# Optimization experiments

Measured on AMD Instinct MI355X. Metric: run time of the kernel, lower is better.

Reference implementation:

```python
import jax, jax.numpy as jnp
import numpy as np

N = 50000   # nodes
E = 800000  # edges
B = 64      # graphs in batch
IN = 128    # in_features
HID = 64    # hidden_channels
H = 4       # head_count
C = 10      # out_classes
NEG = 0.2   # leaky relu negative slope
EPS = 1e-5  # batchnorm eps (eval mode, running mean 0 / var 1)


def _gat(x, edge_index, W, a_src, a_dst, b):
    """PyG GATConv (add_self_loops=False, concat=True), eval mode (no dropout)."""
    Hh, F = a_src.shape
    xW = (x @ W).reshape(-1, Hh, F)                       # [N,H,F]
    src, dst = edge_index[0], edge_index[1]
    e = (jnp.einsum('nhf,hf->nh', xW, a_src)[src]
         + jnp.einsum('nhf,hf->nh', xW, a_dst)[dst])      # [E,H]
    e = jnp.where(e > 0, e, NEG * e)                      # leaky relu
    m = jax.ops.segment_max(e, dst, num_segments=N)       # per-dst max
    m = jnp.where(jnp.isfinite(m), m, 0.0)
    p = jnp.exp(e - m[dst])
    denom = jax.ops.segment_sum(p, dst, num_segments=N)
    alpha = p / jnp.maximum(denom[dst], 1e-16)            # edge softmax over dst
    out = jax.ops.segment_sum(alpha[:, :, None] * xW[src], dst, num_segments=N)
    return out.reshape(-1, Hh * F) + b


def _bn_relu(y, g, be):
    # BatchNorm1d in eval mode with running_mean=0, running_var=1, then ReLU
    return jax.nn.relu(g * y / jnp.sqrt(1.0 + EPS) + be)


def setup_inputs():
    key = jax.random.key(0)
    ks = jax.random.split(key, 24)
    s = lambda k, shape: (jax.random.normal(k, shape, jnp.float32) * 0.05)
    z = lambda shape: jnp.zeros(shape, jnp.float32)
    o = lambda shape: jnp.ones(shape, jnp.float32)
    return {
        'acc_flag': 0,
        'x': jax.random.normal(ks[0], (N, IN), jnp.float32),
        'edge_index': jax.random.randint(ks[1], (2, E), 0, N),
        'batch': jnp.sort(jax.random.randint(ks[2], (N,), 0, B)),
        # layer 1: GATConv(IN -> HID, heads=H, concat)
        'W1': s(ks[3], (IN, H * HID)), 'a_src1': s(ks[4], (H, HID)), 'a_dst1': s(ks[5], (H, HID)), 'b1': z((H * HID,)),
        # proj: GATConv(H*HID -> HID, heads=1) + BN
        'W2': s(ks[6], (H * HID, HID)), 'a_src2': s(ks[7], (1, HID)), 'a_dst2': s(ks[8], (1, HID)), 'b2': z((HID,)), 'g2': o((HID,)), 'be2': z((HID,)),
        # block 1
        'W3': s(ks[9], (HID, HID)), 'a_src3': s(ks[10], (1, HID)), 'a_dst3': s(ks[11], (1, HID)), 'b3': z((HID,)), 'g3': o((HID,)), 'be3': z((HID,)),
        # block 2
        'W4': s(ks[12], (HID, HID)), 'a_src4': s(ks[13], (1, HID)), 'a_dst4': s(ks[14], (1, HID)), 'b4': z((HID,)), 'g4': o((HID,)), 'be4': z((HID,)),
        # MLP head
        'Wh1': s(ks[15], (HID, 128)), 'bh1': z((128,)),
        'Wh2': s(ks[16], (128, C)), 'bh2': z((C,)),
    }


def reference(acc_flag, x, edge_index, batch,
              W1, a_src1, a_dst1, b1,
              W2, a_src2, a_dst2, b2, g2, be2,
              W3, a_src3, a_dst3, b3, g3, be3,
              W4, a_src4, a_dst4, b4, g4, be4,
              Wh1, bh1, Wh2, bh2):
    # hardware GAT layer + ReLU (relu applied twice in original -> idempotent)
    x1 = jax.nn.relu(_gat(x, edge_index, W1, a_src1, a_dst1, b1))   # [N, H*HID]
    # projection block: residual base is zeros (shape mismatch H*HID vs HID)
    h = _bn_relu(_gat(x1, edge_index, W2, a_src2, a_dst2, b2), g2, be2)
    # residual blocks (shapes match -> x + relu(bn(y)))
    h = h + _bn_relu(_gat(h, edge_index, W3, a_src3, a_dst3, b3), g3, be3)
    h = h + _bn_relu(_gat(h, edge_index, W4, a_src4, a_dst4, b4), g4, be4)
    # global mean pool over graphs
    pooled = jax.ops.segment_sum(h, batch, num_segments=B)
    cnt = jnp.maximum(jax.ops.segment_sum(jnp.ones((N,), h.dtype), batch, num_segments=B), 1.0)
    hp = pooled / cnt[:, None]                                      # [B, HID]
    # MLP head
    return jax.nn.relu(hp @ Wh1 + bh1) @ Wh2 + bh2                  # [B, C]
```

## Files before the change

kernel.cpp:

```cpp
#include <hip/hip_runtime.h>

#define N_NODES 50000
#define N_EDGES 800000
#define N_GRAPHS 64
#define F_IN 128
#define F_HID 64
#define N_HEADS 4
#define N_CLASSES 10
#define NEG_SLOPE 0.2f
#define BN_RSQ 0.9999950000374997f

typedef __bf16 bf16x8 __attribute__((ext_vector_type(8)));
typedef float floatx4 __attribute__((ext_vector_type(4)));

__device__ __forceinline__ float lrelu(float v) { return v > 0.0f ? v : NEG_SLOPE * v; }

__device__ __forceinline__ float b2f(unsigned short u) {
    return __uint_as_float(((unsigned int)u) << 16);
}
__device__ __forceinline__ unsigned short f2b(float f) {
    unsigned int u = __float_as_uint(f);
    return (unsigned short)((u + 0x7fffu + ((u >> 16) & 1u)) >> 16);
}
__device__ __forceinline__ float blo(unsigned int d) { return __uint_as_float(d << 16); }
__device__ __forceinline__ float bhi(unsigned int d) { return __uint_as_float(d & 0xffff0000u); }

__global__ void k_deg(const int* __restrict__ ei, int* __restrict__ deg) {
    int e = blockIdx.x * blockDim.x + threadIdx.x;
    if (e < N_EDGES) atomicAdd(&deg[ei[N_EDGES + e]], 1);
}

__global__ void k_offs(const int* __restrict__ deg, int* __restrict__ offs,
                       int* __restrict__ total) {
    int i = blockIdx.x * blockDim.x + threadIdx.x;
    int lane = threadIdx.x & 63;
    int v = (i < N_NODES) ? deg[i] : 0;
    int incl = v;
    for (int o = 1; o < 64; o <<= 1) {
        int t = __shfl_up(incl, o);
        if (lane >= o) incl += t;
    }
    int wtot = __shfl(incl, 63);
    int base = 0;
    if (lane == 0) base = atomicAdd(total, wtot);
    base = __shfl(base, 0);
    if (i < N_NODES) offs[i] = base + incl - v;
}

__global__ void k_fill(const int* __restrict__ ei, const int* __restrict__ offs,
                       int* __restrict__ cur, int* __restrict__ csr_src) {
    int e = blockIdx.x * blockDim.x + threadIdx.x;
    if (e < N_EDGES) {
        int d = ei[N_EDGES + e];
        int pos = offs[d] + atomicAdd(&cur[d], 1);
        csr_src[pos] = ei[e];
    }
}

__global__ void k_bounds(const int* __restrict__ batch, int* __restrict__ bounds) {
    int g = threadIdx.x;
    if (g > N_GRAPHS) return;
    int lo = 0, hi = N_NODES;
    while (lo < hi) {
        int mid = (lo + hi) >> 1;
        if (batch[mid] < g) lo = mid + 1; else hi = mid;
    }
    bounds[g] = lo;
}

__global__ void k_prepw(const float* __restrict__ W, unsigned short* __restrict__ Wt,
                        int K, int N) {
    int i = blockIdx.x * blockDim.x + threadIdx.x;
    if (i < K * N) {
        int k = i / N, n = i % N;
        Wt[n * K + k] = f2b(W[i]);
    }
}

template <int K, int N, int HEADS, bool AF32>
__global__ __launch_bounds__(256) void k_mgemm(const void* __restrict__ Ap,
                                               const unsigned short* __restrict__ Bt,
                                               const float* __restrict__ asrc,
                                               const float* __restrict__ adst,
                                               unsigned short* __restrict__ out,
                                               float* __restrict__ es,
                                               float* __restrict__ ed, int rows) {
    constexpr int LDP = K + 8;
    __shared__ unsigned short As[64 * LDP];
    const int tid = threadIdx.x;
    const int r0 = blockIdx.x * 64;
    if (AF32) {
        const float* A = (const float*)Ap;
        for (int i = tid; i < 16 * K; i += 256) {
            int r = i / (K / 4), c4 = i % (K / 4);
            int row = r0 + r;
            float4 v = (row < rows) ? *(const float4*)&A[(size_t)row * K + c4 * 4]
                                    : make_float4(0.f, 0.f, 0.f, 0.f);
            ushort4 u;
            u.x = f2b(v.x); u.y = f2b(v.y); u.z = f2b(v.z); u.w = f2b(v.w);
            *(ushort4*)&As[r * LDP + c4 * 4] = u;
        }
    } else {
        const unsigned short* A = (const unsigned short*)Ap;
        for (int i = tid; i < 8 * K; i += 256) {
            int r = i / (K / 8), c8 = i % (K / 8);
            int row = r0 + r;
            uint4 v;
            if (row < rows) v = *(const uint4*)&A[(size_t)row * K + c8 * 8];
            else { v.x = v.y = v.z = v.w = 0; }
            *(uint4*)&As[r * LDP + c8 * 8] = v;
        }
    }
    __syncthreads();
    const int w = tid >> 6, lane = tid & 63;
    const int quad = lane >> 4, l16 = lane & 15;
    const int gr0 = r0 + w * 16 + quad * 4;
    bf16x8 afrag[K / 32];
#pragma unroll
    for (int kk = 0; kk < K / 32; ++kk)
        afrag[kk] = *(const bf16x8*)&As[(w * 16 + l16) * LDP + kk * 32 + quad * 8];
    float sacc[4] = {0.f, 0.f, 0.f, 0.f};
    float dacc[4] = {0.f, 0.f, 0.f, 0.f};
#pragma unroll 1
    for (int ct = 0; ct < N / 16; ++ct) {
        floatx4 acc = {0.f, 0.f, 0.f, 0.f};
#pragma unroll
        for (int kk = 0; kk < K / 32; ++kk) {
            const bf16x8 bfrag =
                *(const bf16x8*)&Bt[(size_t)(ct * 16 + l16) * K + kk * 32 + quad * 8];
            acc = __builtin_amdgcn_mfma_f32_16x16x32_bf16(afrag[kk], bfrag, acc, 0, 0, 0);
        }
        const int gc = ct * 16 + l16;
        const int hh = gc >> 6;
        const float av = asrc[gc & (64 * HEADS > N ? N - 1 : 63) + (hh << 6) - (hh << 6)
                              ];
        (void)av;
        {
            const int f = gc & 63;
            const float as = asrc[hh * 64 + f];
            const float ad = adst[hh * 64 + f];
#pragma unroll
            for (int rg = 0; rg < 4; ++rg) {
                sacc[rg] = fmaf(acc[rg], as, sacc[rg]);
                dacc[rg] = fmaf(acc[rg], ad, dacc[rg]);
            }
        }
#pragma unroll
        for (int rg = 0; rg < 4; ++rg) {
            int gr = gr0 + rg;
            if (gr < rows) out[(size_t)gr * N + gc] = f2b(acc[rg]);
        }
        if ((ct & 3) == 3) {
#pragma unroll
            for (int rg = 0; rg < 4; ++rg) {
                float s = sacc[rg], d = dacc[rg];
                for (int o = 1; o < 16; o <<= 1) {
                    s += __shfl_xor(s, o);
                    d += __shfl_xor(d, o);
                }
                if (l16 == 0) {
                    int gr = gr0 + rg;
                    if (gr < rows) {
                        es[(size_t)gr * HEADS + hh] = s;
                        ed[(size_t)gr * HEADS + hh] = d;
                    }
                }
                sacc[rg] = 0.f;
                dacc[rg] = 0.f;
            }
        }
    }
}

__global__ __launch_bounds__(256) void k_gat1(
    const unsigned short* __restrict__ xW, const float* __restrict__ es, const float* __restrict__ ed,
    const int* __restrict__ offs, const int* __restrict__ deg, const int* __restrict__ csr,
    const float* __restrict__ bias, unsigned short* __restrict__ out) {
    __shared__ float ps[4][256];
    __shared__ int sbuf[4][64];
    const int wv = threadIdx.x >> 6;
    const int lane = threadIdx.x & 63;
    const int n = blockIdx.x * 4 + wv;
    if (n >= N_NODES) return;
    const int off = offs[n];
    const int dg = deg[n];
    const float4 edv = *(const float4*)&ed[n * 4];
    const int t = lane & 15, grp = lane >> 4, hq = t >> 2;

    float acc[16];
#pragma unroll
    for (int k = 0; k < 16; ++k) acc[k] = 0.f;
    float d0 = 0.f, d1 = 0.f, d2 = 0.f, d3 = 0.f;

    for (int base = 0; base < dg; base += 64) {
        const int idx = base + lane;
        int s_l = 0;
        float p0 = 0.f, p1 = 0.f, p2 = 0.f, p3 = 0.f;
        if (idx < dg) {
            s_l = csr[off + idx];
            const float4 ev = *(const float4*)&es[s_l * 4];
            p0 = __expf(lrelu(ev.x + edv.x));
            p1 = __expf(lrelu(ev.y + edv.y));
            p2 = __expf(lrelu(ev.z + edv.z));
            p3 = __expf(lrelu(ev.w + edv.w));
        }
        d0 += p0; d1 += p1; d2 += p2; d3 += p3;
        *(float4*)&ps[wv][lane * 4] = make_float4(p0, p1, p2, p3);
        sbuf[wv][lane] = s_l;
        const int cnt = min(64, dg - base);
        const int cntR = (cnt + 7) & ~7;
        for (int j4 = 0; j4 < cntR; j4 += 8) {
            const int ja = j4 + grp;
            const int jb = ja + 4;
            const float pa = ps[wv][ja * 4 + hq];
            const float pb = ps[wv][jb * 4 + hq];
            const int sa = sbuf[wv][ja];
            const int sb = sbuf[wv][jb];
            const uint4 a0 = *(const uint4*)&xW[(size_t)sa * 256 + t * 16];
            const uint4 a1 = *(const uint4*)&xW[(size_t)sa * 256 + t * 16 + 8];
            const uint4 b0 = *(const uint4*)&xW[(size_t)sb * 256 + t * 16];
            const uint4 b1 = *(const uint4*)&xW[(size_t)sb * 256 + t * 16 + 8];
            acc[0]  = fmaf(pa, blo(a0.x), acc[0]);
            acc[1]  = fmaf(pa, bhi(a0.x), acc[1]);
            acc[2]  = fmaf(pa, blo(a0.y), acc[2]);
            acc[3]  = fmaf(pa, bhi(a0.y), acc[3]);
            acc[4]  = fmaf(pa, blo(a0.z), acc[4]);
            acc[5]  = fmaf(pa, bhi(a0.z), acc[5]);
            acc[6]  = fmaf(pa, blo(a0.w), acc[6]);
            acc[7]  = fmaf(pa, bhi(a0.w), acc[7]);
            acc[8]  = fmaf(pa, blo(a1.x), acc[8]);
            acc[9]  = fmaf(pa, bhi(a1.x), acc[9]);
            acc[10] = fmaf(pa, blo(a1.y), acc[10]);
            acc[11] = fmaf(pa, bhi(a1.y), acc[11]);
            acc[12] = fmaf(pa, blo(a1.z), acc[12]);
            acc[13] = fmaf(pa, bhi(a1.z), acc[13]);
            acc[14] = fmaf(pa, blo(a1.w), acc[14]);
            acc[15] = fmaf(pa, bhi(a1.w), acc[15]);
            acc[0]  = fmaf(pb, blo(b0.x), acc[0]);
            acc[1]  = fmaf(pb, bhi(b0.x), acc[1]);
            acc[2]  = fmaf(pb, blo(b0.y), acc[2]);
            acc[3]  = fmaf(pb, bhi(b0.y), acc[3]);
            acc[4]  = fmaf(pb, blo(b0.z), acc[4]);
            acc[5]  = fmaf(pb, bhi(b0.z), acc[5]);
            acc[6]  = fmaf(pb, blo(b0.w), acc[6]);
            acc[7]  = fmaf(pb, bhi(b0.w), acc[7]);
            acc[8]  = fmaf(pb, blo(b1.x), acc[8]);
            acc[9]  = fmaf(pb, bhi(b1.x), acc[9]);
            acc[10] = fmaf(pb, blo(b1.y), acc[10]);
            acc[11] = fmaf(pb, bhi(b1.y), acc[11]);
            acc[12] = fmaf(pb, blo(b1.z), acc[12]);
            acc[13] = fmaf(pb, bhi(b1.z), acc[13]);
            acc[14] = fmaf(pb, blo(b1.w), acc[14]);
            acc[15] = fmaf(pb, bhi(b1.w), acc[15]);
        }
    }
#pragma unroll
    for (int k = 0; k < 16; ++k) {
        acc[k] += __shfl_xor(acc[k], 16);
        acc[k] += __shfl_xor(acc[k], 32);
    }
    for (int o = 1; o < 64; o <<= 1) {
        d0 += __shfl_xor(d0, o);
        d1 += __shfl_xor(d1, o);
        d2 += __shfl_xor(d2, o);
        d3 += __shfl_xor(d3, o);
    }
    if (grp == 0) {
        const float dsel = hq == 0 ? d0 : hq == 1 ? d1 : hq == 2 ? d2 : d3;
        const float inv = 1.0f / fmaxf(dsel, 1e-16f);
#pragma unroll
        for (int k4 = 0; k4 < 16; k4 += 4) {
            const int c = t * 16 + k4;
            const float4 bv = *(const float4*)&bias[c];
            ushort4 o4;
            o4.x = f2b(fmaxf(fmaf(acc[k4 + 0], inv, bv.x), 0.f));
            o4.y = f2b(fmaxf(fmaf(acc[k4 + 1], inv, bv.y), 0.f));
            o4.z = f2b(fmaxf(fmaf(acc[k4 + 2], inv, bv.z), 0.f));
            o4.w = f2b(fmaxf(fmaf(acc[k4 + 3], inv, bv.w), 0.f));
            *(ushort4*)&out[(size_t)n * 256 + c] = o4;
        }
    }
}

template <bool RES>
__global__ __launch_bounds__(256) void k_gatL(
    const unsigned short* __restrict__ xW, const float* __restrict__ es, const float* __restrict__ ed,
    const int* __restrict__ offs, const int* __restrict__ deg, const int* __restrict__ csr,
    const float* __restrict__ bias, const float* __restrict__ gam, const float* __restrict__ bet,
    float* __restrict__ h, unsigned short* __restrict__ hb) {
    __shared__ float ps[4][64];
    __shared__ int sbuf[4][64];
    const int wv = threadIdx.x >> 6;
    const int lane = threadIdx.x & 63;
    const int n = blockIdx.x * 4 + wv;
    if (n >= N_NODES) return;
    const int off = offs[n];
    const int dg = deg[n];
    const float edn = ed[n];
    const int t = lane & 7, grp = lane >> 3;

    float acc[8];
#pragma unroll
    for (int k = 0; k < 8; ++k) acc[k] = 0.f;
    float dsum = 0.f;

    for (int base = 0; base < dg; base += 64) {
        const int idx = base + lane;
        int s_l = 0;
        float p_l = 0.f;
        if (idx < dg) {
            s_l = csr[off + idx];
            p_l = __expf(lrelu(es[s_l] + edn));
        }
        dsum += p_l;
        ps[wv][lane] = p_l;
        sbuf[wv][lane] = s_l;
        const int cnt = min(64, dg - base);
        const int cntR = (cnt + 15) & ~15;
        for (int j8 = 0; j8 < cntR; j8 += 16) {
            const int ja = j8 + grp;
            const int jb = ja + 8;
            const float pa = ps[wv][ja];
            const float pb = ps[wv][jb];
            const int sa = sbuf[wv][ja];
            const int sb = sbuf[wv][jb];
            const uint4 a = *(const uint4*)&xW[(size_t)sa * 64 + t * 8];
            const uint4 b = *(const uint4*)&xW[(size_t)sb * 64 + t * 8];
            acc[0] = fmaf(pa, blo(a.x), acc[0]);
            acc[1] = fmaf(pa, bhi(a.x), acc[1]);
            acc[2] = fmaf(pa, blo(a.y), acc[2]);
            acc[3] = fmaf(pa, bhi(a.y), acc[3]);
            acc[4] = fmaf(pa, blo(a.z), acc[4]);
            acc[5] = fmaf(pa, bhi(a.z), acc[5]);
            acc[6] = fmaf(pa, blo(a.w), acc[6]);
            acc[7] = fmaf(pa, bhi(a.w), acc[7]);
            acc[0] = fmaf(pb, blo(b.x), acc[0]);
            acc[1] = fmaf(pb, bhi(b.x), acc[1]);
            acc[2] = fmaf(pb, blo(b.y), acc[2]);
            acc[3] = fmaf(pb, bhi(b.y), acc[3]);
            acc[4] = fmaf(pb, blo(b.z), acc[4]);
            acc[5] = fmaf(pb, bhi(b.z), acc[5]);
            acc[6] = fmaf(pb, blo(b.w), acc[6]);
            acc[7] = fmaf(pb, bhi(b.w), acc[7]);
        }
    }
#pragma unroll
    for (int k = 0; k < 8; ++k) {
        acc[k] += __shfl_xor(acc[k], 8);
        acc[k] += __shfl_xor(acc[k], 16);
        acc[k] += __shfl_xor(acc[k], 32);
    }
    for (int o = 1; o < 64; o <<= 1) dsum += __shfl_xor(dsum, o);

    if (grp == 0) {
        const float inv = 1.0f / fmaxf(dsum, 1e-16f);
        const int c0 = t * 8;
        float hn[8];
#pragma unroll
        for (int k = 0; k < 8; ++k) {
            const int c = c0 + k;
            const float y = fmaf(acc[k], inv, bias[c]);
            const float z = fmaxf(fmaf(gam[c] * y, BN_RSQ, bet[c]), 0.f);
            hn[k] = RES ? h[(size_t)n * 64 + c] + z : z;
        }
        *(float4*)&h[(size_t)n * 64 + c0] = make_float4(hn[0], hn[1], hn[2], hn[3]);
        *(float4*)&h[(size_t)n * 64 + c0 + 4] = make_float4(hn[4], hn[5], hn[6], hn[7]);
        ushort4 u0, u1;
        u0.x = f2b(hn[0]); u0.y = f2b(hn[1]); u0.z = f2b(hn[2]); u0.w = f2b(hn[3]);
        u1.x = f2b(hn[4]); u1.y = f2b(hn[5]); u1.z = f2b(hn[6]); u1.w = f2b(hn[7]);
        *(ushort4*)&hb[(size_t)n * 64 + c0] = u0;
        *(ushort4*)&hb[(size_t)n * 64 + c0 + 4] = u1;
    }
}

__global__ __launch_bounds__(256) void k_pool2(const float* __restrict__ h,
                                               const int* __restrict__ bounds,
                                               float* __restrict__ hp) {
    __shared__ float part[4][64];
    const int g = blockIdx.x;
    const int lane = threadIdx.x & 63;
    const int wid = threadIdx.x >> 6;
    const int s = bounds[g], e = bounds[g + 1];
    float acc = 0.f;
    for (int n = s + wid; n < e; n += 4) acc += h[n * 64 + lane];
    part[wid][lane] = acc;
    __syncthreads();
    if (wid == 0) {
        float v = part[0][lane] + part[1][lane] + part[2][lane] + part[3][lane];
        hp[g * 64 + lane] = v / fmaxf((float)(e - s), 1.0f);
    }
}

__global__ __launch_bounds__(256) void k_head(const float* __restrict__ hpg,
                                              const float* __restrict__ Wh1,
                                              const float* __restrict__ bh1,
                                              const float* __restrict__ Wh2,
                                              const float* __restrict__ bh2,
                                              float* __restrict__ out) {
    __shared__ float hp[64 * 64];
    __shared__ float t1[64 * 128];
    const int tid = threadIdx.x;
    for (int i = tid; i < 64 * 64; i += 256) hp[i] = hpg[i];
    __syncthreads();
    for (int i = tid; i < 64 * 128; i += 256) {
        int g = i >> 7, j = i & 127;
        float s = bh1[j];
        for (int k = 0; k < 64; ++k) s = fmaf(hp[g * 64 + k], Wh1[k * 128 + j], s);
        t1[i] = fmaxf(s, 0.f);
    }
    __syncthreads();
    for (int i = tid; i < 640; i += 256) {
        int g = i / 10, j = i - g * 10;
        float s = bh2[j];
        for (int k = 0; k < 128; ++k) s = fmaf(t1[g * 128 + k], Wh2[k * 10 + j], s);
        out[i] = s;
    }
}

extern "C" void kernel_launch(void* const* d_in, const int* in_sizes, int n_in,
                              void* d_out, int out_size, void* d_ws, size_t ws_size,
                              hipStream_t stream) {
    const float* x = (const float*)d_in[1];
    const int* ei = (const int*)d_in[2];
    const int* batch = (const int*)d_in[3];
    const float* W1 = (const float*)d_in[4];
    const float* a_src1 = (const float*)d_in[5];
    const float* a_dst1 = (const float*)d_in[6];
    const float* b1 = (const float*)d_in[7];
    const float* W2 = (const float*)d_in[8];
    const float* a_src2 = (const float*)d_in[9];
    const float* a_dst2 = (const float*)d_in[10];
    const float* b2 = (const float*)d_in[11];
    const float* g2 = (const float*)d_in[12];
    const float* be2 = (const float*)d_in[13];
    const float* W3 = (const float*)d_in[14];
    const float* a_src3 = (const float*)d_in[15];
    const float* a_dst3 = (const float*)d_in[16];
    const float* b3 = (const float*)d_in[17];
    const float* g3 = (const float*)d_in[18];
    const float* be3 = (const float*)d_in[19];
    const float* W4 = (const float*)d_in[20];
    const float* a_src4 = (const float*)d_in[21];
    const float* a_dst4 = (const float*)d_in[22];
    const float* b4 = (const float*)d_in[23];
    const float* g4 = (const float*)d_in[24];
    const float* be4 = (const float*)d_in[25];
    const float* Wh1 = (const float*)d_in[26];
    const float* bh1 = (const float*)d_in[27];
    const float* Wh2 = (const float*)d_in[28];
    const float* bh2 = (const float*)d_in[29];
    float* out = (float*)d_out;

    char* p = (char*)d_ws;
    auto alloc = [&](size_t bytes) {
        void* r = (void*)p;
        p += (bytes + 255) & ~(size_t)255;
        return r;
    };
    unsigned short* bufA = (unsigned short*)alloc((size_t)N_NODES * 256 * 2);
    unsigned short* x1b = (unsigned short*)alloc((size_t)N_NODES * 256 * 2);
    float* h = (float*)alloc((size_t)N_NODES * 64 * 4);
    unsigned short* hb = (unsigned short*)alloc((size_t)N_NODES * 64 * 2);
    float* es1 = (float*)alloc((size_t)N_NODES * 4 * 4);
    float* ed1 = (float*)alloc((size_t)N_NODES * 4 * 4);
    float* esL = (float*)alloc((size_t)N_NODES * 4);
    float* edL = (float*)alloc((size_t)N_NODES * 4);
    int* offs = (int*)alloc((size_t)N_NODES * 4);
    int* csr = (int*)alloc((size_t)N_EDGES * 4);
    int* bounds = (int*)alloc((size_t)(N_GRAPHS + 1) * 4);
    float* hpool = (float*)alloc((size_t)N_GRAPHS * 64 * 4);
    unsigned short* Wt1 = (unsigned short*)alloc((size_t)128 * 256 * 2);
    unsigned short* Wt2 = (unsigned short*)alloc((size_t)256 * 64 * 2);
    unsigned short* Wt3 = (unsigned short*)alloc((size_t)64 * 64 * 2);
    unsigned short* Wt4 = (unsigned short*)alloc((size_t)64 * 64 * 2);
    char* z0 = p;
    int* deg = (int*)alloc((size_t)N_NODES * 4);
    int* cur = (int*)alloc((size_t)N_NODES * 4);
    int* total = (int*)alloc(256);
    size_t zbytes = (size_t)(p - z0);
    hipMemsetAsync(z0, 0, zbytes, stream);

    const int edgeBlocks = (N_EDGES + 255) / 256;
    const int nodeBlocks = (N_NODES + 255) / 256;
    const int mgemmBlocks = (N_NODES + 63) / 64;
    const int gatBlocks = (N_NODES + 3) / 4;

    k_prepw<<<(128 * 256 + 255) / 256, 256, 0, stream>>>(W1, Wt1, 128, 256);
    k_prepw<<<(256 * 64 + 255) / 256, 256, 0, stream>>>(W2, Wt2, 256, 64);
    k_prepw<<<(64 * 64 + 255) / 256, 256, 0, stream>>>(W3, Wt3, 64, 64);
    k_prepw<<<(64 * 64 + 255) / 256, 256, 0, stream>>>(W4, Wt4, 64, 64);

    k_deg<<<edgeBlocks, 256, 0, stream>>>(ei, deg);
    k_offs<<<nodeBlocks, 256, 0, stream>>>(deg, offs, total);
    k_fill<<<edgeBlocks, 256, 0, stream>>>(ei, offs, cur, csr);
    k_bounds<<<1, 128, 0, stream>>>(batch, bounds);

    k_mgemm<128, 256, 4, true><<<mgemmBlocks, 256, 0, stream>>>(x, Wt1, a_src1, a_dst1,
                                                                bufA, es1, ed1, N_NODES);
    k_gat1<<<gatBlocks, 256, 0, stream>>>(bufA, es1, ed1, offs, deg, csr, b1, x1b);

    k_mgemm<256, 64, 1, false><<<mgemmBlocks, 256, 0, stream>>>(x1b, Wt2, a_src2, a_dst2,
                                                                bufA, esL, edL, N_NODES);
    k_gatL<false><<<gatBlocks, 256, 0, stream>>>(bufA, esL, edL, offs, deg, csr, b2, g2, be2, h, hb);

    k_mgemm<64, 64, 1, false><<<mgemmBlocks, 256, 0, stream>>>(hb, Wt3, a_src3, a_dst3,
                                                               bufA, esL, edL, N_NODES);
    k_gatL<true><<<gatBlocks, 256, 0, stream>>>(bufA, esL, edL, offs, deg, csr, b3, g3, be3, h, hb);

    k_mgemm<64, 64, 1, false><<<mgemmBlocks, 256, 0, stream>>>(hb, Wt4, a_src4, a_dst4,
                                                               bufA, esL, edL, N_NODES);
    k_gatL<true><<<gatBlocks, 256, 0, stream>>>(bufA, esL, edL, offs, deg, csr, b4, g4, be4, h, hb);

    k_pool2<<<N_GRAPHS, 256, 0, stream>>>(h, bounds, hpool);
    k_head<<<1, 256, 0, stream>>>(hpool, Wh1, bh1, Wh2, bh2, out);
}
```

Before: 543.5 us.

## Split each GAT node across two waves and merge small setup kernels

```diff
diff --git a/kernel.cpp b/kernel.cpp
--- a/kernel.cpp
+++ b/kernel.cpp
@@ -3,10 +3,6 @@
 #define N_NODES 50000
 #define N_EDGES 800000
 #define N_GRAPHS 64
-#define F_IN 128
-#define F_HID 64
-#define N_HEADS 4
-#define N_CLASSES 10
 #define NEG_SLOPE 0.2f
 #define BN_RSQ 0.9999950000374997f
 
@@ -31,7 +27,17 @@
 }
 
 __global__ void k_offs(const int* __restrict__ deg, int* __restrict__ offs,
-                       int* __restrict__ total) {
+                       int* __restrict__ total, const int* __restrict__ batch,
+                       int* __restrict__ bounds) {
+    if (blockIdx.x == 0 && threadIdx.x <= N_GRAPHS) {
+        int g = threadIdx.x;
+        int lo = 0, hi = N_NODES;
+        while (lo < hi) {
+            int mid = (lo + hi) >> 1;
+            if (batch[mid] < g) lo = mid + 1; else hi = mid;
+        }
+        bounds[g] = lo;
+    }
     int i = blockIdx.x * blockDim.x + threadIdx.x;
     int lane = threadIdx.x & 63;
     int v = (i < N_NODES) ? deg[i] : 0;
@@ -57,23 +63,26 @@
     }
 }
 
-__global__ void k_bounds(const int* __restrict__ batch, int* __restrict__ bounds) {
-    int g = threadIdx.x;
-    if (g > N_GRAPHS) return;
-    int lo = 0, hi = N_NODES;
-    while (lo < hi) {
-        int mid = (lo + hi) >> 1;
-        if (batch[mid] < g) lo = mid + 1; else hi = mid;
-    }
-    bounds[g] = lo;
-}
-
-__global__ void k_prepw(const float* __restrict__ W, unsigned short* __restrict__ Wt,
-                        int K, int N) {
+__global__ void k_prepw(const float* __restrict__ W1, const float* __restrict__ W2,
+                        const float* __restrict__ W3, const float* __restrict__ W4,
+                        unsigned short* __restrict__ Wt1, unsigned short* __restrict__ Wt2,
+                        unsigned short* __restrict__ Wt3, unsigned short* __restrict__ Wt4) {
     int i = blockIdx.x * blockDim.x + threadIdx.x;
-    if (i < K * N) {
-        int k = i / N, n = i % N;
-        Wt[n * K + k] = f2b(W[i]);
+    if (i < 32768) {
+        int k = i >> 8, n = i & 255;
+        Wt1[n * 128 + k] = f2b(W1[i]);
+    } else if (i < 49152) {
+        int j = i - 32768;
+        int k = j >> 6, n = j & 63;
+        Wt2[n * 256 + k] = f2b(W2[j]);
+    } else if (i < 53248) {
+        int j = i - 49152;
+        int k = j >> 6, n = j & 63;
+        Wt3[n * 64 + k] = f2b(W3[j]);
+    } else if (i < 57344) {
+        int j = i - 53248;
+        int k = j >> 6, n = j & 63;
+        Wt4[n * 64 + k] = f2b(W4[j]);
     }
 }
 
@@ -132,18 +141,13 @@
         }
         const int gc = ct * 16 + l16;
         const int hh = gc >> 6;
-        const float av = asrc[gc & (64 * HEADS > N ? N - 1 : 63) + (hh << 6) - (hh << 6)
-                              ];
-        (void)av;
-        {
-            const int f = gc & 63;
-            const float as = asrc[hh * 64 + f];
-            const float ad = adst[hh * 64 + f];
-#pragma unroll
-            for (int rg = 0; rg < 4; ++rg) {
-                sacc[rg] = fmaf(acc[rg], as, sacc[rg]);
-                dacc[rg] = fmaf(acc[rg], ad, dacc[rg]);
-            }
+        const int f = gc & 63;
+        const float as = asrc[hh * 64 + f];
+        const float ad = adst[hh * 64 + f];
+#pragma unroll
+        for (int rg = 0; rg < 4; ++rg) {
+            sacc[rg] = fmaf(acc[rg], as, sacc[rg]);
+            dacc[rg] = fmaf(acc[rg], ad, dacc[rg]);
         }
 #pragma unroll
         for (int rg = 0; rg < 4; ++rg) {
@@ -176,109 +180,114 @@
     const unsigned short* __restrict__ xW, const float* __restrict__ es, const float* __restrict__ ed,
     const int* __restrict__ offs, const int* __restrict__ deg, const int* __restrict__ csr,
     const float* __restrict__ bias, unsigned short* __restrict__ out) {
-    __shared__ float ps[4][256];
+    __shared__ float ps[4][128];
     __shared__ int sbuf[4][64];
     const int wv = threadIdx.x >> 6;
     const int lane = threadIdx.x & 63;
-    const int n = blockIdx.x * 4 + wv;
+    const int n = blockIdx.x * 2 + (wv >> 1);
+    const int half = wv & 1;
     if (n >= N_NODES) return;
     const int off = offs[n];
     const int dg = deg[n];
-    const float4 edv = *(const float4*)&ed[n * 4];
-    const int t = lane & 15, grp = lane >> 4, hq = t >> 2;
-
-    float acc[16];
-#pragma unroll
-    for (int k = 0; k < 16; ++k) acc[k] = 0.f;
-    float d0 = 0.f, d1 = 0.f, d2 = 0.f, d3 = 0.f;
+    const float2 edv = *(const float2*)&ed[n * 4 + half * 2];
+    const int t = lane & 15, grp = lane >> 4;
+    const int hsel = t >> 3;
+
+    float acc[8];
+#pragma unroll
+    for (int k = 0; k < 8; ++k) acc[k] = 0.f;
+    float dA = 0.f, dB = 0.f;
 
     for (int base = 0; base < dg; base += 64) {
         const int idx = base + lane;
         int s_l = 0;
-        float p0 = 0.f, p1 = 0.f, p2 = 0.f, p3 = 0.f;
+        float pA = 0.f, pB = 0.f;
         if (idx < dg) {
             s_l = csr[off + idx];
-            const float4 ev = *(const float4*)&es[s_l * 4];
-            p0 = __expf(lrelu(ev.x + edv.x));
-            p1 = __expf(lrelu(ev.y + edv.y));
-            p2 = __expf(lrelu(ev.z + edv.z));
-            p3 = __expf(lrelu(ev.w + edv.w));
-        }
-        d0 += p0; d1 += p1; d2 += p2; d3 += p3;
-        *(float4*)&ps[wv][lane * 4] = make_float4(p0, p1, p2, p3);
+            const float2 ev = *(const float2*)&es[s_l * 4 + half * 2];
+            pA = __expf(lrelu(ev.x + edv.x));
+            pB = __expf(lrelu(ev.y + edv.y));
+        }
+        dA += pA; dB += pB;
+        *(float2*)&ps[wv][lane * 2] = make_float2(pA, pB);
         sbuf[wv][lane] = s_l;
         const int cnt = min(64, dg - base);
-        const int cntR = (cnt + 7) & ~7;
-        for (int j4 = 0; j4 < cntR; j4 += 8) {
-            const int ja = j4 + grp;
-            const int jb = ja + 4;
-            const float pa = ps[wv][ja * 4 + hq];
-            const float pb = ps[wv][jb * 4 + hq];
-            const int sa = sbuf[wv][ja];
-            const int sb = sbuf[wv][jb];
-            const uint4 a0 = *(const uint4*)&xW[(size_t)sa * 256 + t * 16];
-            const uint4 a1 = *(const uint4*)&xW[(size_t)sa * 256 + t * 16 + 8];
-            const uint4 b0 = *(const uint4*)&xW[(size_t)sb * 256 + t * 16];
-            const uint4 b1 = *(const uint4*)&xW[(size_t)sb * 256 + t * 16 + 8];
-            acc[0]  = fmaf(pa, blo(a0.x), acc[0]);
-            acc[1]  = fmaf(pa, bhi(a0.x), acc[1]);
-            acc[2]  = fmaf(pa, blo(a0.y), acc[2]);
-            acc[3]  = fmaf(pa, bhi(a0.y), acc[3]);
-            acc[4]  = fmaf(pa, blo(a0.z), acc[4]);
-            acc[5]  = fmaf(pa, bhi(a0.z), acc[5]);
-            acc[6]  = fmaf(pa, blo(a0.w), acc[6]);
-            acc[7]  = fmaf(pa, bhi(a0.w), acc[7]);
-            acc[8]  = fmaf(pa, blo(a1.x), acc[8]);
-            acc[9]  = fmaf(pa, bhi(a1.x), acc[9]);
-            acc[10] = fmaf(pa, blo(a1.y), acc[10]);
-            acc[11] = fmaf(pa, bhi(a1.y), acc[11]);
-            acc[12] = fmaf(pa, blo(a1.z), acc[12]);
-            acc[13] = fmaf(pa, bhi(a1.z), acc[13]);
-            acc[14] = fmaf(pa, blo(a1.w), acc[14]);
-            acc[15] = fmaf(pa, bhi(a1.w), acc[15]);
-            acc[0]  = fmaf(pb, blo(b0.x), acc[0]);
-            acc[1]  = fmaf(pb, bhi(b0.x), acc[1]);
-            acc[2]  = fmaf(pb, blo(b0.y), acc[2]);
-            acc[3]  = fmaf(pb, bhi(b0.y), acc[3]);
-            acc[4]  = fmaf(pb, blo(b0.z), acc[4]);
-            acc[5]  = fmaf(pb, bhi(b0.z), acc[5]);
-            acc[6]  = fmaf(pb, blo(b0.w), acc[6]);
-            acc[7]  = fmaf(pb, bhi(b0.w), acc[7]);
-            acc[8]  = fmaf(pb, blo(b1.x), acc[8]);
-            acc[9]  = fmaf(pb, bhi(b1.x), acc[9]);
-            acc[10] = fmaf(pb, blo(b1.y), acc[10]);
-            acc[11] = fmaf(pb, bhi(b1.y), acc[11]);
-            acc[12] = fmaf(pb, blo(b1.z), acc[12]);
-            acc[13] = fmaf(pb, bhi(b1.z), acc[13]);
-            acc[14] = fmaf(pb, blo(b1.w), acc[14]);
-            acc[15] = fmaf(pb, bhi(b1.w), acc[15]);
-        }
-    }
-#pragma unroll
-    for (int k = 0; k < 16; ++k) {
+        const int cntR = (cnt + 15) & ~15;
+        for (int j0 = 0; j0 < cntR; j0 += 16) {
+            const int j = j0 + grp;
+            const float p0 = ps[wv][j * 2 + hsel];
+            const float p1 = ps[wv][(j + 4) * 2 + hsel];
+            const float p2 = ps[wv][(j + 8) * 2 + hsel];
+            const float p3 = ps[wv][(j + 12) * 2 + hsel];
+            const int s0 = sbuf[wv][j];
+            const int s1 = sbuf[wv][j + 4];
+            const int s2 = sbuf[wv][j + 8];
+            const int s3 = sbuf[wv][j + 12];
+            const int c0 = half * 128 + t * 8;
+            const uint4 a0 = *(const uint4*)&xW[(size_t)s0 * 256 + c0];
+            const uint4 a1 = *(const uint4*)&xW[(size_t)s1 * 256 + c0];
+            const uint4 a2 = *(const uint4*)&xW[(size_t)s2 * 256 + c0];
+            const uint4 a3 = *(const uint4*)&xW[(size_t)s3 * 256 + c0];
+            acc[0] = fmaf(p0, blo(a0.x), acc[0]);
+            acc[1] = fmaf(p0, bhi(a0.x), acc[1]);
+            acc[2] = fmaf(p0, blo(a0.y), acc[2]);
+            acc[3] = fmaf(p0, bhi(a0.y), acc[3]);
+            acc[4] = fmaf(p0, blo(a0.z), acc[4]);
+            acc[5] = fmaf(p0, bhi(a0.z), acc[5]);
+            acc[6] = fmaf(p0, blo(a0.w), acc[6]);
+            acc[7] = fmaf(p0, bhi(a0.w), acc[7]);
+            acc[0] = fmaf(p1, blo(a1.x), acc[0]);
+            acc[1] = fmaf(p1, bhi(a1.x), acc[1]);
+            acc[2] = fmaf(p1, blo(a1.y), acc[2]);
+            acc[3] = fmaf(p1, bhi(a1.y), acc[3]);
+            acc[4] = fmaf(p1, blo(a1.z), acc[4]);
+            acc[5] = fmaf(p1, bhi(a1.z), acc[5]);
+            acc[6] = fmaf(p1, blo(a1.w), acc[6]);
+            acc[7] = fmaf(p1, bhi(a1.w), acc[7]);
+            acc[0] = fmaf(p2, blo(a2.x), acc[0]);
+            acc[1] = fmaf(p2, bhi(a2.x), acc[1]);
+            acc[2] = fmaf(p2, blo(a2.y), acc[2]);
+            acc[3] = fmaf(p2, bhi(a2.y), acc[3]);
+            acc[4] = fmaf(p2, blo(a2.z), acc[4]);
+            acc[5] = fmaf(p2, bhi(a2.z), acc[5]);
+            acc[6] = fmaf(p2, blo(a2.w), acc[6]);
+            acc[7] = fmaf(p2, bhi(a2.w), acc[7]);
+            acc[0] = fmaf(p3, blo(a3.x), acc[0]);
+            acc[1] = fmaf(p3, bhi(a3.x), acc[1]);
+            acc[2] = fmaf(p3, blo(a3.y), acc[2]);
+            acc[3] = fmaf(p3, bhi(a3.y), acc[3]);
+            acc[4] = fmaf(p3, blo(a3.z), acc[4]);
+            acc[5] = fmaf(p3, bhi(a3.z), acc[5]);
+            acc[6] = fmaf(p3, blo(a3.w), acc[6]);
+            acc[7] = fmaf(p3, bhi(a3.w), acc[7]);
+        }
+    }
+#pragma unroll
+    for (int k = 0; k < 8; ++k) {
         acc[k] += __shfl_xor(acc[k], 16);
         acc[k] += __shfl_xor(acc[k], 32);
     }
     for (int o = 1; o < 64; o <<= 1) {
-        d0 += __shfl_xor(d0, o);
-        d1 += __shfl_xor(d1, o);
-        d2 += __shfl_xor(d2, o);
-        d3 += __shfl_xor(d3, o);
+        dA += __shfl_xor(dA, o);
+        dB += __shfl_xor(dB, o);
     }
     if (grp == 0) {
-        const float dsel = hq == 0 ? d0 : hq == 1 ? d1 : hq == 2 ? d2 : d3;
+        const float dsel = hsel == 0 ? dA : dB;
         const float inv = 1.0f / fmaxf(dsel, 1e-16f);
-#pragma unroll
-        for (int k4 = 0; k4 < 16; k4 += 4) {
-            const int c = t * 16 + k4;
-            const float4 bv = *(const float4*)&bias[c];
-            ushort4 o4;
-            o4.x = f2b(fmaxf(fmaf(acc[k4 + 0], inv, bv.x), 0.f));
-            o4.y = f2b(fmaxf(fmaf(acc[k4 + 1], inv, bv.y), 0.f));
-            o4.z = f2b(fmaxf(fmaf(acc[k4 + 2], inv, bv.z), 0.f));
-            o4.w = f2b(fmaxf(fmaf(acc[k4 + 3], inv, bv.w), 0.f));
-            *(ushort4*)&out[(size_t)n * 256 + c] = o4;
-        }
+        const int c0 = half * 128 + t * 8;
+        const float4 bv0 = *(const float4*)&bias[c0];
+        const float4 bv1 = *(const float4*)&bias[c0 + 4];
+        ushort4 o0, o1;
+        o0.x = f2b(fmaxf(fmaf(acc[0], inv, bv0.x), 0.f));
+        o0.y = f2b(fmaxf(fmaf(acc[1], inv, bv0.y), 0.f));
+        o0.z = f2b(fmaxf(fmaf(acc[2], inv, bv0.z), 0.f));
+        o0.w = f2b(fmaxf(fmaf(acc[3], inv, bv0.w), 0.f));
+        o1.x = f2b(fmaxf(fmaf(acc[4], inv, bv1.x), 0.f));
+        o1.y = f2b(fmaxf(fmaf(acc[5], inv, bv1.y), 0.f));
+        o1.z = f2b(fmaxf(fmaf(acc[6], inv, bv1.z), 0.f));
+        o1.w = f2b(fmaxf(fmaf(acc[7], inv, bv1.w), 0.f));
+        *(ushort4*)&out[(size_t)n * 256 + c0] = o0;
+        *(ushort4*)&out[(size_t)n * 256 + c0 + 4] = o1;
     }
 }
 
@@ -292,16 +301,17 @@
     __shared__ int sbuf[4][64];
     const int wv = threadIdx.x >> 6;
     const int lane = threadIdx.x & 63;
-    const int n = blockIdx.x * 4 + wv;
+    const int n = blockIdx.x * 2 + (wv >> 1);
+    const int half = wv & 1;
     if (n >= N_NODES) return;
     const int off = offs[n];
     const int dg = deg[n];
     const float edn = ed[n];
     const int t = lane & 7, grp = lane >> 3;
 
-    float acc[8];
-#pragma unroll
-    for (int k = 0; k < 8; ++k) acc[k] = 0.f;
+    float acc[4];
+#pragma unroll
+    for (int k = 0; k < 4; ++k) acc[k] = 0.f;
     float dsum = 0.f;
 
     for (int base = 0; base < dg; base += 64) {
@@ -317,35 +327,28 @@
         sbuf[wv][lane] = s_l;
         const int cnt = min(64, dg - base);
         const int cntR = (cnt + 15) & ~15;
-        for (int j8 = 0; j8 < cntR; j8 += 16) {
-            const int ja = j8 + grp;
+        for (int j0 = 0; j0 < cntR; j0 += 16) {
+            const int ja = j0 + grp;
             const int jb = ja + 8;
             const float pa = ps[wv][ja];
             const float pb = ps[wv][jb];
             const int sa = sbuf[wv][ja];
             const int sb = sbuf[wv][jb];
-            const uint4 a = *(const uint4*)&xW[(size_t)sa * 64 + t * 8];
-            const uint4 b = *(const uint4*)&xW[(size_t)sb * 64 + t * 8];
+            const int c0 = half * 32 + t * 4;
+            const uint2 a = *(const uint2*)&xW[(size_t)sa * 64 + c0];
+            const uint2 b = *(const uint2*)&xW[(size_t)sb * 64 + c0];
             acc[0] = fmaf(pa, blo(a.x), acc[0]);
             acc[1] = fmaf(pa, bhi(a.x), acc[1]);
             acc[2] = fmaf(pa, blo(a.y), acc[2]);
             acc[3] = fmaf(pa, bhi(a.y), acc[3]);
-            acc[4] = fmaf(pa, blo(a.z), acc[4]);
-            acc[5] = fmaf(pa, bhi(a.z), acc[5]);
-            acc[6] = fmaf(pa, blo(a.w), acc[6]);
-            acc[7] = fmaf(pa, bhi(a.w), acc[7]);
             acc[0] = fmaf(pb, blo(b.x), acc[0]);
             acc[1] = fmaf(pb, bhi(b.x), acc[1]);
             acc[2] = fmaf(pb, blo(b.y), acc[2]);
             acc[3] = fmaf(pb, bhi(b.y), acc[3]);
-            acc[4] = fmaf(pb, blo(b.z), acc[4]);
-            acc[5] = fmaf(pb, bhi(b.z), acc[5]);
-            acc[6] = fmaf(pb, blo(b.w), acc[6]);
-            acc[7] = fmaf(pb, bhi(b.w), acc[7]);
-        }
-    }
-#pragma unroll
-    for (int k = 0; k < 8; ++k) {
+        }
+    }
+#pragma unroll
+    for (int k = 0; k < 4; ++k) {
         acc[k] += __shfl_xor(acc[k], 8);
         acc[k] += __shfl_xor(acc[k], 16);
         acc[k] += __shfl_xor(acc[k], 32);
@@ -354,22 +357,19 @@
 
     if (grp == 0) {
         const float inv = 1.0f / fmaxf(dsum, 1e-16f);
-        const int c0 = t * 8;
-        float hn[8];
-#pragma unroll
-        for (int k = 0; k < 8; ++k) {
+        const int c0 = half * 32 + t * 4;
+        float hn[4];
+#pragma unroll
+        for (int k = 0; k < 4; ++k) {
             const int c = c0 + k;
             const float y = fmaf(acc[k], inv, bias[c]);
             const float z = fmaxf(fmaf(gam[c] * y, BN_RSQ, bet[c]), 0.f);
             hn[k] = RES ? h[(size_t)n * 64 + c] + z : z;
         }
         *(float4*)&h[(size_t)n * 64 + c0] = make_float4(hn[0], hn[1], hn[2], hn[3]);
-        *(float4*)&h[(size_t)n * 64 + c0 + 4] = make_float4(hn[4], hn[5], hn[6], hn[7]);
-        ushort4 u0, u1;
-        u0.x = f2b(hn[0]); u0.y = f2b(hn[1]); u0.z = f2b(hn[2]); u0.w = f2b(hn[3]);
-        u1.x = f2b(hn[4]); u1.y = f2b(hn[5]); u1.z = f2b(hn[6]); u1.w = f2b(hn[7]);
-        *(ushort4*)&hb[(size_t)n * 64 + c0] = u0;
-        *(ushort4*)&hb[(size_t)n * 64 + c0 + 4] = u1;
+        ushort4 u;
+        u.x = f2b(hn[0]); u.y = f2b(hn[1]); u.z = f2b(hn[2]); u.w = f2b(hn[3]);
+        *(ushort4*)&hb[(size_t)n * 64 + c0] = u;
     }
 }
 
@@ -483,17 +483,13 @@
     const int edgeBlocks = (N_EDGES + 255) / 256;
     const int nodeBlocks = (N_NODES + 255) / 256;
     const int mgemmBlocks = (N_NODES + 63) / 64;
-    const int gatBlocks = (N_NODES + 3) / 4;
-
-    k_prepw<<<(128 * 256 + 255) / 256, 256, 0, stream>>>(W1, Wt1, 128, 256);
-    k_prepw<<<(256 * 64 + 255) / 256, 256, 0, stream>>>(W2, Wt2, 256, 64);
-    k_prepw<<<(64 * 64 + 255) / 256, 256, 0, stream>>>(W3, Wt3, 64, 64);
-    k_prepw<<<(64 * 64 + 255) / 256, 256, 0, stream>>>(W4, Wt4, 64, 64);
+    const int gatBlocks = (N_NODES + 1) / 2;
+
+    k_prepw<<<(57344 + 255) / 256, 256, 0, stream>>>(W1, W2, W3, W4, Wt1, Wt2, Wt3, Wt4);
 
     k_deg<<<edgeBlocks, 256, 0, stream>>>(ei, deg);
-    k_offs<<<nodeBlocks, 256, 0, stream>>>(deg, offs, total);
+    k_offs<<<nodeBlocks, 256, 0, stream>>>(deg, offs, total, batch, bounds);
     k_fill<<<edgeBlocks, 256, 0, stream>>>(ei, offs, cur, csr);
-    k_bounds<<<1, 128, 0, stream>>>(batch, bounds);
 
     k_mgemm<128, 256, 4, true><<<mgemmBlocks, 256, 0, stream>>>(x, Wt1, a_src1, a_dst1,
                                                                 bufA, es1, ed1, N_NODES);
```

After: 582.0 us. +7.1%, slower.
